# Optimization experiments

Measured on AMD Instinct MI355X. Metric: run time of the kernel, lower is better.

Reference implementation:

```python
import jax, jax.numpy as jnp
import numpy as np

PI = np.float32(np.pi)


def _normal(v):
    return v / jnp.linalg.norm(v, axis=-1, keepdims=True)


def camera_mats(cameras):
    # cameras: [V,5] -> rotation matrices c: [V,3,3], camera origins o: [V,3]
    theta = cameras[:, 0] * (PI / 180.0)
    phi = cameras[:, 1] * (PI / 180.0)
    camy = cameras[:, 3] * jnp.sin(phi)
    lens = cameras[:, 3] * jnp.cos(phi)
    camx = lens * jnp.cos(theta)
    camz = lens * jnp.sin(theta)
    Zax = jnp.stack([camx, camy, camz], -1)                                   # [V,3]
    Yax = jnp.stack([camy * jnp.cos(theta + PI), lens, camy * jnp.sin(theta + PI)], -1)
    Xax = jnp.cross(Yax, Zax)
    c = jnp.stack([_normal(Xax), _normal(Yax), _normal(Zax)], axis=1)         # [V,3,3]
    return c, Zax


def setup_inputs() -> dict:
    key = jax.random.key(0)
    k0, k1, k2, k3, k4, k5 = jax.random.split(key, 6)
    N = 65536
    return {
        "inputs": jax.random.normal(k0, (N, 3), jnp.float32),
        "cameras": jax.random.uniform(k1, (3, 5), jnp.float32),
        "feat0": jax.random.normal(k2, (3, 64, 56, 56), jnp.float32),
        "feat1": jax.random.normal(k3, (3, 128, 28, 28), jnp.float32),
        "feat2": jax.random.normal(k4, (3, 256, 14, 14), jnp.float32),
        "feat3": jax.random.normal(k5, (3, 512, 7, 7), jnp.float32),
    }


def reference(inputs, cameras, feat0, feat1, feat2, feat3):
    V = 3
    N = inputs.shape[0]
    c, o = camera_mats(cameras)                      # [V,3,3], [V,3]
    # camera_trans_inv with view 0: xyz @ inv(c0.T) + o0
    point_origin = inputs @ jnp.linalg.inv(c[0].T) + o[0]          # [N,3]
    # camera_trans per view: (p - o_v) @ c_v.T
    pts = jnp.einsum('vnd,vkd->vnk', point_origin[None, :, :] - o[:, None, :], c)  # [V,N,3]
    X, Y, Z = pts[..., 0], pts[..., 1], pts[..., 2]
    h = jnp.clip(jnp.nan_to_num(248.0 * (-Y) / (-Z) + 112.0), 0.0, 223.0)
    w = jnp.clip(jnp.nan_to_num(248.0 * X / (-Z) + 112.0), 0.0, 223.0)
    n = jnp.broadcast_to(jnp.arange(V, dtype=jnp.float32)[:, None], (V, N))
    indices = jnp.stack([n, h, w], axis=-1)                        # [V,N,3] float

    def gather(feat, size):
        # faithful: n is also divided and truncated -> batch index always 0
        idx = (indices / (224.0 / size)).astype(jnp.int32)         # [V,N,3]
        f = jnp.transpose(feat, (0, 2, 3, 1))                      # [B,H,W,C]
        return f[idx[..., 0], idx[..., 1], idx[..., 2]]            # [V,N,C]

    image_feature = jnp.concatenate(
        [gather(feat0, 56.0), gather(feat1, 28.0), gather(feat2, 14.0), gather(feat3, 7.0)],
        axis=2)                                                    # [V,N,960]
    fmax = jnp.max(image_feature, axis=0)
    fmean = jnp.mean(image_feature, axis=0)
    fstd = jnp.sqrt(jnp.mean((image_feature - fmean) ** 2, axis=0))  # biased std
    return jnp.concatenate([inputs, fmax, fmean, fstd], axis=1)    # [N, 3+3*960]
```

## Files before the change

kernel.cpp:

```cpp
#include <hip/hip_runtime.h>
#include <math.h>


#define TBL_TOTAL 376320
#define TBL_OFF0  0
#define TBL_OFF1  200704
#define TBL_OFF2  301056
#define TBL_OFF3  351232

__device__ __forceinline__ void compute_cams(const float* __restrict__ cams,
                                             double M[3][3], double o0[3],
                                             double cm[3][3][3], double om[3][3]) {
  const double DEG  = (double)(3.14159274101257324f / 180.0f);
  const double PI_D = (double)3.14159274101257324f;
  for (int v = 0; v < 3; ++v) {
    double th = (double)cams[v * 5 + 0] * DEG;
    double ph = (double)cams[v * 5 + 1] * DEG;
    double dd = (double)cams[v * 5 + 3];
    double camy = dd * sin(ph);
    double lens = dd * cos(ph);
    double camx = lens * cos(th);
    double camz = lens * sin(th);
    double Zx = camx, Zy = camy, Zz = camz;
    double Yx = camy * cos(th + PI_D), Yy = lens, Yz = camy * sin(th + PI_D);
    double Xx = Yy * Zz - Yz * Zy;
    double Xy = Yz * Zx - Yx * Zz;
    double Xz = Yx * Zy - Yy * Zx;
    double nX = sqrt(Xx * Xx + Xy * Xy + Xz * Xz);
    double nY = sqrt(Yx * Yx + Yy * Yy + Yz * Yz);
    double nZ = sqrt(Zx * Zx + Zy * Zy + Zz * Zz);
    cm[v][0][0] = Xx / nX; cm[v][0][1] = Xy / nX; cm[v][0][2] = Xz / nX;
    cm[v][1][0] = Yx / nY; cm[v][1][1] = Yy / nY; cm[v][1][2] = Yz / nY;
    cm[v][2][0] = Zx / nZ; cm[v][2][1] = Zy / nZ; cm[v][2][2] = Zz / nZ;
    om[v][0] = Zx; om[v][1] = Zy; om[v][2] = Zz;
  }
  double a00 = cm[0][0][0], a01 = cm[0][1][0], a02 = cm[0][2][0];
  double a10 = cm[0][0][1], a11 = cm[0][1][1], a12 = cm[0][2][1];
  double a20 = cm[0][0][2], a21 = cm[0][1][2], a22 = cm[0][2][2];
  double det = a00 * (a11 * a22 - a12 * a21)
             - a01 * (a10 * a22 - a12 * a20)
             + a02 * (a10 * a21 - a11 * a20);
  M[0][0] = (a11 * a22 - a12 * a21) / det;
  M[0][1] = (a02 * a21 - a01 * a22) / det;
  M[0][2] = (a01 * a12 - a02 * a11) / det;
  M[1][0] = (a12 * a20 - a10 * a22) / det;
  M[1][1] = (a00 * a22 - a02 * a20) / det;
  M[1][2] = (a02 * a10 - a00 * a12) / det;
  M[2][0] = (a10 * a21 - a11 * a20) / det;
  M[2][1] = (a01 * a20 - a00 * a21) / det;
  M[2][2] = (a00 * a11 - a01 * a10) / det;
  o0[0] = om[0][0]; o0[1] = om[0][1]; o0[2] = om[0][2];
}

__global__ void k_setup(const float* __restrict__ cams, double* __restrict__ P) {
  if (threadIdx.x != 0 || blockIdx.x != 0) return;
  double M[3][3], o0[3], cm[3][3][3], om[3][3];
  compute_cams(cams, M, o0, cm, om);
  int i = 0;
  for (int r = 0; r < 3; ++r)
    for (int k = 0; k < 3; ++k) P[i++] = M[r][k];
  for (int k = 0; k < 3; ++k) P[i++] = o0[k];
  for (int v = 0; v < 3; ++v)
    for (int r = 0; r < 3; ++r)
      for (int k = 0; k < 3; ++k) P[i++] = cm[v][r][k];
  for (int v = 0; v < 3; ++v)
    for (int k = 0; k < 3; ++k) P[i++] = om[v][k];
}

__global__ void k_transpose(const float* __restrict__ f0, const float* __restrict__ f1,
                            const float* __restrict__ f2, const float* __restrict__ f3,
                            float* __restrict__ tbl) {
  int i = blockIdx.x * 256 + threadIdx.x;
  if (i >= TBL_TOTAL) return;
  const float* src;
  int j, cmask, clog, HW;
  if (i < TBL_OFF1)      { src = f0; j = i;            cmask = 63;  clog = 6; HW = 3136; }
  else if (i < TBL_OFF2) { src = f1; j = i - TBL_OFF1; cmask = 127; clog = 7; HW = 784;  }
  else if (i < TBL_OFF3) { src = f2; j = i - TBL_OFF2; cmask = 255; clog = 8; HW = 196;  }
  else                   { src = f3; j = i - TBL_OFF3; cmask = 511; clog = 9; HW = 49;   }
  int c  = j & cmask;
  int hw = j >> clog;
  tbl[i] = src[c * HW + hw];
}

template <bool TRANSPOSED>
__global__ __launch_bounds__(256) void k_main(
    const float* __restrict__ inpts, const float* __restrict__ cams,
    const double* __restrict__ P, const float* __restrict__ tbl,
    const float* __restrict__ f0, const float* __restrict__ f1,
    const float* __restrict__ f2, const float* __restrict__ f3,
    float* __restrict__ out) {
  __shared__ int s_off[3][4];
  const int p = blockIdx.x;
  const int tid = threadIdx.x;

  if (tid < 3) {
    const int v = tid;
    double M[3][3], o0[3], cmv[3][3], ovv[3];
    if (TRANSPOSED) {
      M[0][0] = P[0]; M[0][1] = P[1]; M[0][2] = P[2];
      M[1][0] = P[3]; M[1][1] = P[4]; M[1][2] = P[5];
      M[2][0] = P[6]; M[2][1] = P[7]; M[2][2] = P[8];
      o0[0] = P[9]; o0[1] = P[10]; o0[2] = P[11];
      for (int r = 0; r < 3; ++r)
        for (int k = 0; k < 3; ++k) cmv[r][k] = P[12 + v * 9 + r * 3 + k];
      ovv[0] = P[39 + v * 3 + 0]; ovv[1] = P[39 + v * 3 + 1]; ovv[2] = P[39 + v * 3 + 2];
    } else {
      double cm[3][3][3], om[3][3];
      compute_cams(cams, M, o0, cm, om);
      for (int r = 0; r < 3; ++r)
        for (int k = 0; k < 3; ++k) cmv[r][k] = cm[v][r][k];
      ovv[0] = om[v][0]; ovv[1] = om[v][1]; ovv[2] = om[v][2];
    }
    double x = (double)inpts[p * 3 + 0];
    double y = (double)inpts[p * 3 + 1];
    double z = (double)inpts[p * 3 + 2];
    double p0 = x * M[0][0] + y * M[1][0] + z * M[2][0] + o0[0];
    double p1 = x * M[0][1] + y * M[1][1] + z * M[2][1] + o0[1];
    double p2 = x * M[0][2] + y * M[1][2] + z * M[2][2] + o0[2];
    double q0 = p0 - ovv[0], q1 = p1 - ovv[1], q2 = p2 - ovv[2];
    double Xc = q0 * cmv[0][0] + q1 * cmv[0][1] + q2 * cmv[0][2];
    double Yc = q0 * cmv[1][0] + q1 * cmv[1][1] + q2 * cmv[1][2];
    double Zc = q0 * cmv[2][0] + q1 * cmv[2][1] + q2 * cmv[2][2];
    double nz = -Zc;
    double hv = 248.0 * (-Yc) / nz + 112.0;
    double wv = 248.0 * Xc / nz + 112.0;
    if (isnan(hv)) hv = 0.0;
    if (isnan(wv)) wv = 0.0;
    hv = fmin(fmax(hv, 0.0), 223.0);
    wv = fmin(fmax(wv, 0.0), 223.0);
    int h0 = (int)(hv * 0.25),    w0 = (int)(wv * 0.25);
    int h1 = (int)(hv * 0.125),   w1 = (int)(wv * 0.125);
    int h2 = (int)(hv * 0.0625),  w2 = (int)(wv * 0.0625);
    int h3 = (int)(hv * 0.03125), w3 = (int)(wv * 0.03125);
    if (TRANSPOSED) {
      s_off[v][0] = TBL_OFF0 + (h0 * 56 + w0) * 64;
      s_off[v][1] = TBL_OFF1 + (h1 * 28 + w1) * 128;
      s_off[v][2] = TBL_OFF2 + (h2 * 14 + w2) * 256;
      s_off[v][3] = TBL_OFF3 + (h3 * 7  + w3) * 512;
    } else {
      s_off[v][0] = h0 * 56 + w0;
      s_off[v][1] = h1 * 28 + w1;
      s_off[v][2] = h2 * 14 + w2;
      s_off[v][3] = h3 * 7  + w3;
    }
    out[p * 2883 + v] = inpts[p * 3 + v];
  }
  __syncthreads();

  const int row = p * 2883;
  for (int c = tid; c < 960; c += 256) {
    int l, cl;
    if (c < 64)       { l = 0; cl = c; }
    else if (c < 192) { l = 1; cl = c - 64; }
    else if (c < 448) { l = 2; cl = c - 192; }
    else              { l = 3; cl = c - 448; }
    float v0, v1, v2;
    if (TRANSPOSED) {
      v0 = tbl[s_off[0][l] + cl];
      v1 = tbl[s_off[1][l] + cl];
      v2 = tbl[s_off[2][l] + cl];
    } else {
      const float* f = (l == 0) ? f0 : (l == 1) ? f1 : (l == 2) ? f2 : f3;
      const int HW   = (l == 0) ? 3136 : (l == 1) ? 784 : (l == 2) ? 196 : 49;
      v0 = f[cl * HW + s_off[0][l]];
      v1 = f[cl * HW + s_off[1][l]];
      v2 = f[cl * HW + s_off[2][l]];
    }
    float mx = fmaxf(fmaxf(v0, v1), v2);
    float sm = (v0 + v1) + v2;
    float mean = sm / 3.0f;
    float d0 = v0 - mean, d1 = v1 - mean, d2 = v2 - mean;
    float var = ((d0 * d0 + d1 * d1) + d2 * d2) / 3.0f;
    float sd = sqrtf(var);
    out[row + 3 + c]    = mx;
    out[row + 963 + c]  = mean;
    out[row + 1923 + c] = sd;
  }
}

extern "C" void kernel_launch(void* const* d_in, const int* in_sizes, int n_in,
                              void* d_out, int out_size, void* d_ws, size_t ws_size,
                              hipStream_t stream) {
  const float* inpts = (const float*)d_in[0];
  const float* cams  = (const float*)d_in[1];
  const float* f0    = (const float*)d_in[2];
  const float* f1    = (const float*)d_in[3];
  const float* f2    = (const float*)d_in[4];
  const float* f3    = (const float*)d_in[5];
  float* out = (float*)d_out;
  const int N = in_sizes[0] / 3;

  const size_t TBL_BYTE_OFF = 512;
  const size_t NEED = TBL_BYTE_OFF + (size_t)TBL_TOTAL * sizeof(float);

  if (ws_size >= NEED) {
    double* P  = (double*)d_ws;
    float* tbl = (float*)((char*)d_ws + TBL_BYTE_OFF);
    k_setup<<<1, 64, 0, stream>>>(cams, P);
    k_transpose<<<(TBL_TOTAL + 255) / 256, 256, 0, stream>>>(f0, f1, f2, f3, tbl);
    k_main<true><<<N, 256, 0, stream>>>(inpts, cams, P, tbl, f0, f1, f2, f3, out);
  } else {
    k_main<false><<<N, 256, 0, stream>>>(inpts, cams, nullptr, nullptr, f0, f1, f2, f3, out);
  }
}
```

Before: 827.4 us.

## Split per-point geometry into its own kernel and gather one point per wavefront

Adds a k_geom kernel that computes the projected table offsets for every point once, one point per thread, and stores them in the workspace. A new k_gather kernel then handles one point per 64-lane wavefront, four points per block, with unrolled channel loops and nontemporal stores. This removes the per-block __syncthreads and the serial double-precision projection done by three threads while the rest of the block waits. In exchange it needs an extra kernel launch and N*12 ints of workspace, and falls back to the old path if the workspace is too small.

```diff
diff --git a/kernel.cpp b/kernel.cpp
--- a/kernel.cpp
+++ b/kernel.cpp
@@ -81,6 +81,89 @@
   int c  = j & cmask;
   int hw = j >> clog;
   tbl[i] = src[c * HW + hw];
+}
+
+__global__ __launch_bounds__(256) void k_geom(const float* __restrict__ inpts,
+                                              const double* __restrict__ P,
+                                              int* __restrict__ off,
+                                              float* __restrict__ out, int N) {
+  int p = blockIdx.x * 256 + threadIdx.x;
+  if (p >= N) return;
+  double x = (double)inpts[p * 3 + 0];
+  double y = (double)inpts[p * 3 + 1];
+  double z = (double)inpts[p * 3 + 2];
+  double p0 = x * P[0] + y * P[3] + z * P[6] + P[9];
+  double p1 = x * P[1] + y * P[4] + z * P[7] + P[10];
+  double p2 = x * P[2] + y * P[5] + z * P[8] + P[11];
+  int4 r[3];
+  #pragma unroll
+  for (int v = 0; v < 3; ++v) {
+    const double* cmv = P + 12 + v * 9;
+    const double* ovv = P + 39 + v * 3;
+    double q0 = p0 - ovv[0], q1 = p1 - ovv[1], q2 = p2 - ovv[2];
+    double Xc = q0 * cmv[0] + q1 * cmv[1] + q2 * cmv[2];
+    double Yc = q0 * cmv[3] + q1 * cmv[4] + q2 * cmv[5];
+    double Zc = q0 * cmv[6] + q1 * cmv[7] + q2 * cmv[8];
+    double nz = -Zc;
+    double hv = 248.0 * (-Yc) / nz + 112.0;
+    double wv = 248.0 * Xc / nz + 112.0;
+    if (isnan(hv)) hv = 0.0;
+    if (isnan(wv)) wv = 0.0;
+    hv = fmin(fmax(hv, 0.0), 223.0);
+    wv = fmin(fmax(wv, 0.0), 223.0);
+    int h0 = (int)(hv * 0.25),    w0 = (int)(wv * 0.25);
+    int h1 = (int)(hv * 0.125),   w1 = (int)(wv * 0.125);
+    int h2 = (int)(hv * 0.0625),  w2 = (int)(wv * 0.0625);
+    int h3 = (int)(hv * 0.03125), w3 = (int)(wv * 0.03125);
+    r[v].x = TBL_OFF0 + (h0 * 56 + w0) * 64;
+    r[v].y = TBL_OFF1 + (h1 * 28 + w1) * 128;
+    r[v].z = TBL_OFF2 + (h2 * 14 + w2) * 256;
+    r[v].w = TBL_OFF3 + (h3 * 7  + w3) * 512;
+  }
+  int4* op = (int4*)(off + p * 12);
+  op[0] = r[0]; op[1] = r[1]; op[2] = r[2];
+  out[p * 2883 + 0] = inpts[p * 3 + 0];
+  out[p * 2883 + 1] = inpts[p * 3 + 1];
+  out[p * 2883 + 2] = inpts[p * 3 + 2];
+}
+
+__global__ __launch_bounds__(256) void k_gather(const int* __restrict__ off,
+                                                const float* __restrict__ tbl,
+                                                float* __restrict__ out, int N) {
+  const int wid = (blockIdx.x << 2) | (threadIdx.x >> 6);
+  if (wid >= N) return;
+  const int lane = threadIdx.x & 63;
+  const int4* ob = (const int4*)(off + wid * 12);
+  const int4 o0 = ob[0];
+  const int4 o1 = ob[1];
+  const int4 o2 = ob[2];
+  float* __restrict__ row = out + (size_t)wid * 2883;
+
+#define DO64(BASE_C, OO0, OO1, OO2, CL)                         \
+  {                                                             \
+    float v0 = tbl[(OO0) + (CL)];                               \
+    float v1 = tbl[(OO1) + (CL)];                               \
+    float v2 = tbl[(OO2) + (CL)];                               \
+    float mx = fmaxf(fmaxf(v0, v1), v2);                        \
+    float sm = (v0 + v1) + v2;                                  \
+    float mean = sm / 3.0f;                                     \
+    float d0 = v0 - mean, d1 = v1 - mean, d2 = v2 - mean;       \
+    float var = ((d0 * d0 + d1 * d1) + d2 * d2) / 3.0f;         \
+    float sd = sqrtf(var);                                      \
+    int c = (BASE_C) + (CL);                                    \
+    __builtin_nontemporal_store(mx,   row + 3 + c);             \
+    __builtin_nontemporal_store(mean, row + 963 + c);           \
+    __builtin_nontemporal_store(sd,   row + 1923 + c);          \
+  }
+
+  DO64(0, o0.x, o1.x, o2.x, lane);
+  #pragma unroll
+  for (int j = 0; j < 2; ++j) DO64(64, o0.y, o1.y, o2.y, lane + 64 * j);
+  #pragma unroll
+  for (int j = 0; j < 4; ++j) DO64(192, o0.z, o1.z, o2.z, lane + 64 * j);
+  #pragma unroll
+  for (int j = 0; j < 8; ++j) DO64(448, o0.w, o1.w, o2.w, lane + 64 * j);
+#undef DO64
 }
 
 template <bool TRANSPOSED>
@@ -192,9 +275,19 @@
   const int N = in_sizes[0] / 3;
 
   const size_t TBL_BYTE_OFF = 512;
-  const size_t NEED = TBL_BYTE_OFF + (size_t)TBL_TOTAL * sizeof(float);
-
-  if (ws_size >= NEED) {
+  const size_t OFF_BYTE_OFF = TBL_BYTE_OFF + (size_t)TBL_TOTAL * sizeof(float);
+  const size_t NEED_FULL = OFF_BYTE_OFF + (size_t)N * 12 * sizeof(int);
+  const size_t NEED_MID  = TBL_BYTE_OFF + (size_t)TBL_TOTAL * sizeof(float);
+
+  if (ws_size >= NEED_FULL) {
+    double* P  = (double*)d_ws;
+    float* tbl = (float*)((char*)d_ws + TBL_BYTE_OFF);
+    int*   off = (int*)((char*)d_ws + OFF_BYTE_OFF);
+    k_setup<<<1, 64, 0, stream>>>(cams, P);
+    k_transpose<<<(TBL_TOTAL + 255) / 256, 256, 0, stream>>>(f0, f1, f2, f3, tbl);
+    k_geom<<<(N + 255) / 256, 256, 0, stream>>>(inpts, P, off, out, N);
+    k_gather<<<(N + 3) / 4, 256, 0, stream>>>(off, tbl, out, N);
+  } else if (ws_size >= NEED_MID) {
     double* P  = (double*)d_ws;
     float* tbl = (float*)((char*)d_ws + TBL_BYTE_OFF);
     k_setup<<<1, 64, 0, stream>>>(cams, P);
```

After: 946.0 us. 14.3% more time.
